# Kernel optimization log

Hardware: AMD Instinct MI355X
Metric: run time of the kernel (lower is better)

## Reference

```python
import jax, jax.numpy as jnp
import numpy as np

FP8_E4M3_MAX = 448.0  # max representable magnitude in float8_e4m3fn


def setup_inputs() -> dict:
    key = jax.random.key(0)
    k1, k2, k3 = jax.random.split(key, 3)
    n_tokens, d_in, d_out = 8192, 4096, 16384
    x = jax.random.normal(k1, (n_tokens, d_in), dtype=jnp.float32)
    # weight stored in fp8 domain (values stand in for dequantized-by-scale fp8 codes)
    weight = jax.random.normal(k2, (d_out, d_in), dtype=jnp.float32)
    bias = jax.random.normal(k3, (d_out,), dtype=jnp.float32) * 0.1
    input_scale = jnp.float32(0.05)   # per-tensor activation scale
    weight_scale = jnp.float32(0.01)  # per-tensor weight scale
    return {"x": x, "weight": weight, "bias": bias,
            "input_scale": input_scale, "weight_scale": weight_scale}


def reference(x, weight, bias, input_scale, weight_scale):
    # fp8 qdq path: quantize activation to fp8 e4m3 domain (fake-quant: scale + clamp),
    # then scaled GEMM: out = (x_q @ W_q^T) * (input_scale * weight_scale) + bias,
    # matching cublas_scaled_mm(input, weight.t(), scale_a, scale_b) + bias.
    x_q = jnp.clip(x / input_scale, -FP8_E4M3_MAX, FP8_E4M3_MAX)  # [T, d_in]
    acc = jnp.einsum('ti,oi->to', x_q, weight)                     # [T, d_out]
    out = acc * (input_scale * weight_scale) + bias
    return out
```

## Files before the change

kernel.cpp:

```cpp
#include <hip/hip_runtime.h>
#include <stdint.h>
#include <stddef.h>


typedef _Float16 half8 __attribute__((ext_vector_type(8)));
typedef _Float16 half4v __attribute__((ext_vector_type(4)));
typedef float f32x4 __attribute__((ext_vector_type(4)));

#define BM 256
#define BN 256
#define BK 64
#define FP8MAX 448.0f

__device__ __forceinline__ void gload_lds16(const _Float16* g, _Float16* lds) {
  __builtin_amdgcn_global_load_lds(
      (const __attribute__((address_space(1))) uint32_t*)g,
      (__attribute__((address_space(3))) uint32_t*)lds, 16, 0, 0);
}

#define BAR() asm volatile("s_barrier" ::: "memory")
#define WAIT_VM(N) asm volatile("s_waitcnt vmcnt(" #N ")" ::: "memory")
#define WAIT_LGKM(N) asm volatile("s_waitcnt lgkmcnt(" #N ")" ::: "memory")
#define SCHED_FENCE() __builtin_amdgcn_sched_barrier(0)

#define MFMA_Q(AF, BF, MG, NG) do {                                           \
  __builtin_amdgcn_s_setprio(1);                                              \
  _Pragma("unroll")                                                           \
  for (int ks_ = 0; ks_ < 2; ++ks_) {                                         \
    _Pragma("unroll")                                                         \
    for (int mf_ = 0; mf_ < 4; ++mf_) {                                       \
      _Pragma("unroll")                                                       \
      for (int nf_ = 0; nf_ < 2; ++nf_)                                       \
        acc[(MG)*4 + mf_][(NG)*2 + nf_] =                                     \
            __builtin_amdgcn_mfma_f32_16x16x32_f16(                           \
                AF[mf_*2 + ks_], BF[nf_*2 + ks_],                             \
                acc[(MG)*4 + mf_][(NG)*2 + nf_], 0, 0, 0);                    \
    }                                                                         \
  }                                                                           \
  __builtin_amdgcn_s_setprio(0);                                              \
} while (0)

__global__ void cvt_x_kernel(const float* __restrict__ x, _Float16* __restrict__ xq,
                             const float* __restrict__ s_ptr, long n4) {
  float inv = 1.0f / s_ptr[0];
  long i = (long)blockIdx.x * blockDim.x + threadIdx.x;
  long stride = (long)gridDim.x * blockDim.x;
  const float4* x4 = (const float4*)x;
  for (long j = i; j < n4; j += stride) {
    float4 v = x4[j];
    half4v h;
    h[0] = (_Float16)fminf(fmaxf(v.x * inv, -FP8MAX), FP8MAX);
    h[1] = (_Float16)fminf(fmaxf(v.y * inv, -FP8MAX), FP8MAX);
    h[2] = (_Float16)fminf(fmaxf(v.z * inv, -FP8MAX), FP8MAX);
    h[3] = (_Float16)fminf(fmaxf(v.w * inv, -FP8MAX), FP8MAX);
    *(half4v*)(xq + j * 4) = h;
  }
}

__global__ void cvt_w_kernel(const float* __restrict__ w, _Float16* __restrict__ wq,
                             long n4) {
  long i = (long)blockIdx.x * blockDim.x + threadIdx.x;
  long stride = (long)gridDim.x * blockDim.x;
  const float4* w4 = (const float4*)w;
  for (long j = i; j < n4; j += stride) {
    float4 v = w4[j];
    half4v h;
    h[0] = (_Float16)v.x; h[1] = (_Float16)v.y;
    h[2] = (_Float16)v.z; h[3] = (_Float16)v.w;
    *(half4v*)(wq + j * 4) = h;
  }
}

__global__ __launch_bounds__(512, 2)
void gemm256_ko(const _Float16* __restrict__ A, const _Float16* __restrict__ B,
                const float* __restrict__ bias, const float* __restrict__ is_ptr,
                const float* __restrict__ ws_ptr, float* __restrict__ out,
                int M, int N, int K) {
  __shared__ __align__(16) _Float16 sA[2][256 * 64];
  __shared__ __align__(16) _Float16 sB[2][256 * 64];

  const int nbn = N / BN;
  const int nwg = gridDim.x;
  int wg = blockIdx.x;
  if ((nwg & 7) == 0) {
    int q = nwg >> 3;
    wg = (wg & 7) * q + (wg >> 3);
  }
  const int brow = (wg / nbn) * BM;
  const int bcol = (wg % nbn) * BN;

  const int tid  = threadIdx.x;
  const int lane = tid & 63;
  const int w    = tid >> 6;
  const int wr   = w >> 2;
  const int wc   = w & 3;

  const size_t lsrc = (size_t)(lane >> 3) * K + (size_t)((lane & 7) ^ (lane >> 3)) * 8;
  const _Float16* gA = A + (size_t)brow * K + lsrc;
  const _Float16* gB = B + (size_t)bcol * K + lsrc;

  auto stageA = [&](int buf, int pi, int kt) {
    gload_lds16(gA + (size_t)(pi * 64 + w * 8) * K + kt,
                &sA[buf][(pi * 512 + w * 64) * 8]);
  };
  auto stageB = [&](int buf, int pi, int kt) {
    gload_lds16(gB + (size_t)(pi * 64 + w * 8) * K + kt,
                &sB[buf][(pi * 512 + w * 64) * 8]);
  };

  const int rdbase = (lane & 15) * 64;
  const int e0 = rdbase + (((lane >> 4) + 0) ^ (lane & 7)) * 8;
  const int e1 = rdbase + (((lane >> 4) + 4) ^ (lane & 7)) * 8;

  auto ldA = [&](int buf, int mg, half8* a) {
#pragma unroll
    for (int mf = 0; mf < 4; ++mf) {
      const int base = (wr * 8 + mg * 4 + mf) * 1024;
      a[mf * 2 + 0] = *(const half8*)&sA[buf][base + e0];
      a[mf * 2 + 1] = *(const half8*)&sA[buf][base + e1];
    }
  };
  auto ldB = [&](int buf, int ng, half8* b) {
#pragma unroll
    for (int nf = 0; nf < 2; ++nf) {
      const int base = (wc * 4 + ng * 2 + nf) * 1024;
      b[nf * 2 + 0] = *(const half8*)&sB[buf][base + e0];
      b[nf * 2 + 1] = *(const half8*)&sB[buf][base + e1];
    }
  };

  f32x4 acc[8][4] = {};
  const int NT = K / BK;

  stageA(0, 0, 0); stageA(0, 1, 0); stageA(0, 2, 0); stageA(0, 3, 0);
  stageB(0, 0, 0); stageB(0, 1, 0); stageB(0, 2, 0); stageB(0, 3, 0);
  stageA(1, 0, BK); stageA(1, 1, BK); stageA(1, 2, BK); stageA(1, 3, BK);
  WAIT_VM(4);
  BAR();

  for (int t = 0; t < NT; ++t) {
    const int cur = t & 1, nxt = cur ^ 1;
    const int ktB = (t + 1) * BK;
    const int ktA = (t + 2) * BK;
    const bool sb = (t + 1) < NT;
    const bool sa = (t + 2) < NT;
    half8 aL[8], aH[8], bL[4], bH[4];

    ldA(cur, 0, aL); ldB(cur, 0, bL);
    SCHED_FENCE();
    ldB(cur, 1, bH);
    SCHED_FENCE();
    ldA(cur, 1, aH);
    SCHED_FENCE();
    if (sb) { stageB(nxt, 0, ktB); stageB(nxt, 1, ktB);
              stageB(nxt, 2, ktB); stageB(nxt, 3, ktB); }

    WAIT_LGKM(12); SCHED_FENCE();
    MFMA_Q(aL, bL, 0, 0);
    WAIT_LGKM(8); SCHED_FENCE();
    MFMA_Q(aL, bH, 0, 1);
    WAIT_LGKM(0); SCHED_FENCE();
    BAR();

    if (sa) { stageA(cur, 0, ktA); stageA(cur, 1, ktA);
              stageA(cur, 2, ktA); stageA(cur, 3, ktA); }
    MFMA_Q(aH, bH, 1, 1);
    MFMA_Q(aH, bL, 1, 0);

    if (t < NT - 2) { WAIT_VM(4); } else { WAIT_VM(0); }
    BAR();
  }

  const float sc = is_ptr[0] * ws_ptr[0];
  const int orow = brow + wr * 128;
  const int ocol = bcol + wc * 64;
#pragma unroll
  for (int n = 0; n < 4; ++n) {
    const int col = ocol + n * 16 + (lane & 15);
    const float bv = bias[col];
#pragma unroll
    for (int m = 0; m < 8; ++m) {
#pragma unroll
      for (int r = 0; r < 4; ++r) {
        const int row = orow + m * 16 + (lane >> 4) * 4 + r;
        out[(size_t)row * N + col] = acc[m][n][r] * sc + bv;
      }
    }
  }
}

extern "C" void kernel_launch(void* const* d_in, const int* in_sizes, int n_in,
                              void* d_out, int out_size, void* d_ws, size_t ws_size,
                              hipStream_t stream) {
  const float* x    = (const float*)d_in[0];
  const float* wgt  = (const float*)d_in[1];
  const float* bias = (const float*)d_in[2];
  const float* is   = (const float*)d_in[3];
  const float* wsc  = (const float*)d_in[4];
  float* out = (float*)d_out;

  const long x_n = in_sizes[0];
  const long w_n = in_sizes[1];
  const int  N   = in_sizes[2];
  const int  K   = (int)(w_n / N);
  const int  M   = (int)(x_n / K);

  _Float16* xq = (_Float16*)d_ws;
  _Float16* wq = xq + x_n;

  cvt_x_kernel<<<2048, 256, 0, stream>>>(x, xq, is, x_n >> 2);
  cvt_w_kernel<<<2048, 256, 0, stream>>>(wgt, wq, w_n >> 2);

  const int nwg = (M / BM) * (N / BN);
  gemm256_ko<<<nwg, 512, 0, stream>>>(xq, wq, bias, is, wsc, out, M, N, K);
}
```

Measured before the change: 1.197 ms.

## Switch GEMM inner loop to 32x32x16 MFMA with k-step pipelined LDS reads

```diff
diff --git a/kernel.cpp b/kernel.cpp
--- a/kernel.cpp
+++ b/kernel.cpp
@@ -5,7 +5,7 @@
 
 typedef _Float16 half8 __attribute__((ext_vector_type(8)));
 typedef _Float16 half4v __attribute__((ext_vector_type(4)));
-typedef float f32x4 __attribute__((ext_vector_type(4)));
+typedef float f32x16 __attribute__((ext_vector_type(16)));
 
 #define BM 256
 #define BN 256
@@ -23,19 +23,14 @@
 #define WAIT_LGKM(N) asm volatile("s_waitcnt lgkmcnt(" #N ")" ::: "memory")
 #define SCHED_FENCE() __builtin_amdgcn_sched_barrier(0)
 
-#define MFMA_Q(AF, BF, MG, NG) do {                                           \
+#define MFMA_KS(AF, BF) do {                                                  \
   __builtin_amdgcn_s_setprio(1);                                              \
   _Pragma("unroll")                                                           \
-  for (int ks_ = 0; ks_ < 2; ++ks_) {                                         \
+  for (int mb_ = 0; mb_ < 4; ++mb_) {                                         \
     _Pragma("unroll")                                                         \
-    for (int mf_ = 0; mf_ < 4; ++mf_) {                                       \
-      _Pragma("unroll")                                                       \
-      for (int nf_ = 0; nf_ < 2; ++nf_)                                       \
-        acc[(MG)*4 + mf_][(NG)*2 + nf_] =                                     \
-            __builtin_amdgcn_mfma_f32_16x16x32_f16(                           \
-                AF[mf_*2 + ks_], BF[nf_*2 + ks_],                             \
-                acc[(MG)*4 + mf_][(NG)*2 + nf_], 0, 0, 0);                    \
-    }                                                                         \
+    for (int nb_ = 0; nb_ < 2; ++nb_)                                         \
+      acc[mb_][nb_] = __builtin_amdgcn_mfma_f32_32x32x16_f16(                 \
+          AF[mb_], BF[nb_], acc[mb_][nb_], 0, 0, 0);                          \
   }                                                                           \
   __builtin_amdgcn_s_setprio(0);                                              \
 } while (0)
@@ -72,10 +67,10 @@
 }
 
 __global__ __launch_bounds__(512, 2)
-void gemm256_ko(const _Float16* __restrict__ A, const _Float16* __restrict__ B,
-                const float* __restrict__ bias, const float* __restrict__ is_ptr,
-                const float* __restrict__ ws_ptr, float* __restrict__ out,
-                int M, int N, int K) {
+void gemm256_m32(const _Float16* __restrict__ A, const _Float16* __restrict__ B,
+                 const float* __restrict__ bias, const float* __restrict__ is_ptr,
+                 const float* __restrict__ ws_ptr, float* __restrict__ out,
+                 int M, int N, int K) {
   __shared__ __align__(16) _Float16 sA[2][256 * 64];
   __shared__ __align__(16) _Float16 sB[2][256 * 64];
 
@@ -108,28 +103,23 @@
                 &sB[buf][(pi * 512 + w * 64) * 8]);
   };
 
-  const int rdbase = (lane & 15) * 64;
-  const int e0 = rdbase + (((lane >> 4) + 0) ^ (lane & 7)) * 8;
-  const int e1 = rdbase + (((lane >> 4) + 4) ^ (lane & 7)) * 8;
-
-  auto ldA = [&](int buf, int mg, half8* a) {
-#pragma unroll
-    for (int mf = 0; mf < 4; ++mf) {
-      const int base = (wr * 8 + mg * 4 + mf) * 1024;
-      a[mf * 2 + 0] = *(const half8*)&sA[buf][base + e0];
-      a[mf * 2 + 1] = *(const half8*)&sA[buf][base + e1];
-    }
+  const int r31 = (lane & 31) * 64;
+  const int c5  = lane >> 5;
+  const int x7  = lane & 7;
+
+  auto rdks = [&](int buf, int ks, half8 (&af)[4], half8 (&bf)[2]) {
+    const int ch = (((ks << 1) + c5) ^ x7) << 3;
+    const int ea = (wr * 128) * 64 + r31 + ch;
+    const int eb = (wc * 64) * 64 + r31 + ch;
+#pragma unroll
+    for (int mb = 0; mb < 4; ++mb)
+      af[mb] = *(const half8*)&sA[buf][ea + mb * 32 * 64];
+#pragma unroll
+    for (int nb = 0; nb < 2; ++nb)
+      bf[nb] = *(const half8*)&sB[buf][eb + nb * 32 * 64];
   };
-  auto ldB = [&](int buf, int ng, half8* b) {
-#pragma unroll
-    for (int nf = 0; nf < 2; ++nf) {
-      const int base = (wc * 4 + ng * 2 + nf) * 1024;
-      b[nf * 2 + 0] = *(const half8*)&sB[buf][base + e0];
-      b[nf * 2 + 1] = *(const half8*)&sB[buf][base + e1];
-    }
-  };
-
-  f32x4 acc[8][4] = {};
+
+  f32x16 acc[4][2] = {};
   const int NT = K / BK;
 
   stageA(0, 0, 0); stageA(0, 1, 0); stageA(0, 2, 0); stageA(0, 3, 0);
@@ -144,46 +134,51 @@
     const int ktA = (t + 2) * BK;
     const bool sb = (t + 1) < NT;
     const bool sa = (t + 2) < NT;
-    half8 aL[8], aH[8], bL[4], bH[4];
-
-    ldA(cur, 0, aL); ldB(cur, 0, bL);
-    SCHED_FENCE();
-    ldB(cur, 1, bH);
-    SCHED_FENCE();
-    ldA(cur, 1, aH);
+    half8 a0[4], b0[2], a1[4], b1[2];
+
+    rdks(cur, 0, a0, b0);
+    SCHED_FENCE();
+    rdks(cur, 1, a1, b1);
     SCHED_FENCE();
     if (sb) { stageB(nxt, 0, ktB); stageB(nxt, 1, ktB);
               stageB(nxt, 2, ktB); stageB(nxt, 3, ktB); }
 
-    WAIT_LGKM(12); SCHED_FENCE();
-    MFMA_Q(aL, bL, 0, 0);
-    WAIT_LGKM(8); SCHED_FENCE();
-    MFMA_Q(aL, bH, 0, 1);
+    WAIT_LGKM(6); SCHED_FENCE();
+    MFMA_KS(a0, b0);
+    rdks(cur, 2, a0, b0);
+    SCHED_FENCE();
+
+    WAIT_LGKM(6); SCHED_FENCE();
+    MFMA_KS(a1, b1);
+    rdks(cur, 3, a1, b1);
+    SCHED_FENCE();
+
+    WAIT_LGKM(6); SCHED_FENCE();
+    MFMA_KS(a0, b0);
+
     WAIT_LGKM(0); SCHED_FENCE();
     BAR();
-
     if (sa) { stageA(cur, 0, ktA); stageA(cur, 1, ktA);
               stageA(cur, 2, ktA); stageA(cur, 3, ktA); }
-    MFMA_Q(aH, bH, 1, 1);
-    MFMA_Q(aH, bL, 1, 0);
+    MFMA_KS(a1, b1);
 
     if (t < NT - 2) { WAIT_VM(4); } else { WAIT_VM(0); }
     BAR();
   }
 
   const float sc = is_ptr[0] * ws_ptr[0];
-  const int orow = brow + wr * 128;
-  const int ocol = bcol + wc * 64;
-#pragma unroll
-  for (int n = 0; n < 4; ++n) {
-    const int col = ocol + n * 16 + (lane & 15);
+  const int orow = brow + wr * 128 + 4 * c5;
+  const int ocol = bcol + wc * 64 + (lane & 31);
+#pragma unroll
+  for (int nb = 0; nb < 2; ++nb) {
+    const int col = ocol + nb * 32;
     const float bv = bias[col];
 #pragma unroll
-    for (int m = 0; m < 8; ++m) {
-#pragma unroll
-      for (int r = 0; r < 4; ++r) {
-        const int row = orow + m * 16 + (lane >> 4) * 4 + r;
-        out[(size_t)row * N + col] = acc[m][n][r] * sc + bv;
+    for (int mb = 0; mb < 4; ++mb) {
+#pragma unroll
+      for (int r = 0; r < 16; ++r) {
+        const int row = orow + mb * 32 + (r & 3) + 8 * (r >> 2);
+        out[(size_t)row * N + col] = acc[mb][nb][r] * sc + bv;
       }
     }
   }
@@ -212,5 +207,5 @@
   cvt_w_kernel<<<2048, 256, 0, stream>>>(wgt, wq, w_n >> 2);
 
   const int nwg = (M / BM) * (N / BN);
-  gemm256_ko<<<nwg, 512, 0, stream>>>(xq, wq, bias, is, wsc, out, M, N, K);
-}
+  gemm256_m32<<<nwg, 512, 0, stream>>>(xq, wq, bias, is, wsc, out, M, N, K);
+}
```

New measurement: 1.292 ms. 8.0% more time.
